# Kernel tuning notes

Hardware: AMD Instinct MI355X
Metric: run time of the kernel (lower is better)

The kernel has to match this reference:

```python
import jax, jax.numpy as jnp
import numpy as np
from jax import lax

EPS = 1e-05
Q = 4          # window size (hard-coded in BotBlock)
HEADS = 4
DIM = 16       # bottleneck(64) // heads(4)


def conv3x3(x, w, b):
    # x: [N,C,H,W], w: [O,I,3,3]
    y = lax.conv_general_dilated(x, w, (1, 1), ((1, 1), (1, 1)),
                                 dimension_numbers=('NCHW', 'OIHW', 'NCHW'))
    return y + b[None, :, None, None]


def batchnorm(x, gamma, beta):
    # training-mode BN: batch statistics over (N,H,W), biased variance
    m = jnp.mean(x, axis=(0, 2, 3), keepdims=True)
    v = jnp.var(x, axis=(0, 2, 3), keepdims=True)
    xn = (x - m) * lax.rsqrt(v + EPS)
    return xn * gamma[None, :, None, None] + beta[None, :, None, None]


def rel_to_abs(x):
    # x: [B, H, L, 2L-1] -> [B, H, L, L] via pad/reshape trick
    B, H, L, _ = x.shape
    x = jnp.pad(x, ((0, 0), (0, 0), (0, 0), (0, 1)))          # [B,H,L,2L]
    flat = x.reshape(B, H, -1)                                  # [B,H,2L*L]
    flat = jnp.pad(flat, ((0, 0), (0, 0), (0, L - 1)))
    final = flat.reshape(B, H, L + 1, 2 * L - 1)
    return final[:, :, :L, L - 1:]                              # [B,H,L,L]


def relative_logits_1d(q, rel_k, perm):
    # q: [b, n, h, w, d], rel_k: [2w-1, d]
    b, n, h, w, d = q.shape
    rl = jnp.einsum('bnhwd,md->bnhwm', q, rel_k)
    rl = rl.reshape(b, n * h, w, 2 * w - 1)
    rl = rel_to_abs(rl)                                         # [b, n*h, w, w]
    rl = rl.reshape(b, n, h, w, w)
    rl = jnp.broadcast_to(rl[:, :, :, None], (b, n, h, h, w, w))
    return jnp.transpose(rl, perm)


def rel_pos_attention(q, k, v, rel_w, rel_h):
    # q,k,v: [b, heads, h, w, d]
    b, n, h, w, d = q.shape
    q = q * (d ** -0.5)
    logits = jnp.einsum('bnhwd,bnpqd->bnhwpq', q, k)
    logits = logits + relative_logits_1d(q, rel_w, (0, 1, 2, 4, 3, 5))
    logits = logits + relative_logits_1d(jnp.transpose(q, (0, 1, 3, 2, 4)),
                                         rel_h, (0, 1, 4, 2, 5, 3))
    weights = jax.nn.softmax(logits.reshape(b, n, h, w, h * w), axis=-1)
    weights = weights.reshape(b, n, h, w, h, w)
    out = jnp.einsum('bnhwpq,bnpqd->bhwnd', weights, v)         # [b,h,w,n,d]
    return out.reshape(b, h, w, n * d)                          # fold heads


def setup_inputs() -> dict:
    key = jax.random.key(0)
    ks = jax.random.split(key, 16)
    C_in, C_bot, C_out = 64, 64, 256
    inp = {
        'x': jax.random.normal(ks[0], (2, C_in, 256, 256), jnp.float32),
        'conv1_w': jax.random.normal(ks[1], (C_bot, C_in, 3, 3), jnp.float32) * 0.05,
        'conv1_b': jnp.zeros((C_bot,), jnp.float32),
        'bn1_g': jnp.ones((C_bot,), jnp.float32),
        'bn1_b': jnp.zeros((C_bot,), jnp.float32),
        'wq': jax.random.normal(ks[2], (C_bot, HEADS, DIM), jnp.float32) * 0.01,
        'wk': jax.random.normal(ks[3], (C_bot, HEADS, DIM), jnp.float32) * 0.01,
        'wv': jax.random.normal(ks[4], (C_bot, HEADS, DIM), jnp.float32) * 0.01,
        'rel_w': jax.random.normal(ks[5], (2 * Q - 1, DIM), jnp.float32) * (DIM ** -0.5),
        'rel_h': jax.random.normal(ks[6], (2 * Q - 1, DIM), jnp.float32) * (DIM ** -0.5),
        'bn2_g': jnp.ones((C_bot,), jnp.float32),
        'bn2_b': jnp.zeros((C_bot,), jnp.float32),
        'conv3_w': jax.random.normal(ks[7], (C_out, C_bot, 3, 3), jnp.float32) * 0.05,
        'conv3_b': jnp.zeros((C_out,), jnp.float32),
        # NOTE: original init_zero=True zeros bn3 gamma; we randomize it so the
        # output (and gradients) are non-trivial for kernel correctness checks.
        'bn3_g': jax.random.normal(ks[8], (C_out,), jnp.float32),
        'bn3_b': jnp.zeros((C_out,), jnp.float32),
    }
    return inp


def reference(x, conv1_w, conv1_b, bn1_g, bn1_b, wq, wk, wv, rel_w, rel_h,
              bn2_g, bn2_b, conv3_w, conv3_b, bn3_g, bn3_b):
    N, C, H, W = x.shape
    P_h, P_w = H // Q, W // Q
    # raw memory reinterpretation into 4x4 blocks (matches torch .reshape)
    xb = x.reshape(N * P_h * P_w, C, Q, Q)
    out = jax.nn.relu(batchnorm(conv3x3(xb, conv1_w, conv1_b), bn1_g, bn1_b))
    # GroupPointWise projections: NCHW -> NHWC then einsum
    feat = jnp.transpose(out, (0, 2, 3, 1))                     # [b,h,w,c]
    q = jnp.einsum('bhwc,cnp->bnhwp', feat, wq)
    k = jnp.einsum('bhwc,cnp->bnhwp', feat, wk)
    v = jnp.einsum('bhwc,cnp->bnhwp', feat, wv)
    o = rel_pos_attention(q, k, v, rel_w, rel_h)                # [b,h,w,c]
    o = jnp.transpose(o, (0, 3, 1, 2))                          # NCHW
    o = jax.nn.relu(batchnorm(o, bn2_g, bn2_b))
    o = batchnorm(conv3x3(o, conv3_w, conv3_b), bn3_g, bn3_b)   # no act
    C1 = o.shape[1]
    o = o.reshape(N, C1, H, W)
    return jax.nn.relu(o)
```

## Files before the change

kernel.cpp:

```cpp
#include <hip/hip_runtime.h>
#include <stdint.h>


#define EPSV 1e-5f
#define INV_N (1.0f / 131072.0f)

typedef unsigned short u16;
typedef __attribute__((ext_vector_type(8))) short short8b;
typedef __attribute__((ext_vector_type(4))) float f32x4;

__device__ __forceinline__ u16 f2bf(float f) {
  unsigned u = __float_as_uint(f);
  u += 0x7fffu + ((u >> 16) & 1u);
  return (u16)(u >> 16);
}
__device__ __forceinline__ float bf2f(u16 h) {
  return __uint_as_float((unsigned)h << 16);
}

__device__ __forceinline__ float bn_scale(const float* __restrict__ acc,
                                          const float* __restrict__ gam,
                                          const float* __restrict__ bet,
                                          int C, int c, float& shift) {
  float S = acc[c], S2 = acc[C + c];
  float mean = S * INV_N;
  float var  = S2 * INV_N - mean * mean;
  float rstd = rsqrtf(var + EPSV);
  float sc = gam[c] * rstd;
  shift = bet[c] - mean * sc;
  return sc;
}

__global__ __launch_bounds__(256) void prep_kernel(const float* __restrict__ w1,
                                                   const float* __restrict__ w3,
                                                   const float* __restrict__ wq,
                                                   const float* __restrict__ wk,
                                                   const float* __restrict__ wv,
                                                   u16* __restrict__ wp1,
                                                   u16* __restrict__ wp3,
                                                   u16* __restrict__ wqkvT) {
  int i = blockIdx.x * 256 + threadIdx.x;
  const int tot1 = 18 * 64 * 40;
  const int tot3 = 9 * 256 * 64;
  if (i < tot1) {
    int ch = i / (64 * 40); int r = i - ch * 64 * 40; int o = r / 40; int kk = r - o * 40;
    float v = 0.f;
    if (kk < 32) { int k = ch * 32 + kk; int tap = k >> 6; int c = k & 63;
                   v = w1[o * 576 + c * 9 + tap]; }
    wp1[i] = f2bf(v);
  } else if (i < tot1 + tot3) {
    int j = i - tot1;
    int tap = j >> 14; int r = j & 16383; int o = r >> 6; int c = r & 63;
    wp3[j] = f2bf(w3[o * 576 + c * 9 + tap]);
  } else if (i < tot1 + tot3 + 192 * 64) {
    int j = i - tot1 - tot3;
    int oc = j >> 6, c = j & 63;
    const float* src = (oc < 64) ? wq : (oc < 128) ? wk : wv;
    wqkvT[j] = f2bf(src[(c << 6) + (oc & 63)]);
  }
}

__global__ __launch_bounds__(256) void conv1_kernel(const float* __restrict__ x,
                                                    const u16* __restrict__ wp,
                                                    u16* __restrict__ bufb,
                                                    float* __restrict__ partials1) {
  __shared__ __align__(16) char featA[257 * 128];
  __shared__ __align__(16) char ldsW[2][64 * 80];
  const int t = threadIdx.x;
  const int lane = t & 63, w = t >> 6;
  const int lrow = lane & 15, lk = lane >> 4;
  const int wm = w >> 1, wn = w & 1;
  const size_t Mbase = (size_t)blockIdx.x * 256;

  int rel[9];
  {
    const int pi = lrow >> 2, pj = lrow & 3;
#pragma unroll
    for (int tap = 0; tap < 9; ++tap) {
      const int ti = tap / 3, tj = tap - ti * 3;
      int si = pi + ti - 1, sj = pj + tj - 1;
      bool valid = ((unsigned)si < 4u) && ((unsigned)sj < 4u);
      rel[tap] = valid ? ((si * 4 + sj) << 7) : (1 << 24);
    }
  }

#pragma unroll
  for (int i = 0; i < 16; ++i) {
    float4 v = *reinterpret_cast<const float4*>(x + Mbase * 64 + i * 1024 + t * 4);
    const int c = t >> 2, p0 = (t & 3) * 4;
    float vv[4] = {v.x, v.y, v.z, v.w};
#pragma unroll
    for (int j = 0; j < 4; ++j) {
      int row = i * 16 + p0 + j;
      int byte = row * 128 + ((((c >> 3) ^ (row & 7)) << 4) | ((c & 7) << 1));
      *reinterpret_cast<u16*>(featA + byte) = f2bf(vv[j]);
    }
  }
  if (t < 8) *reinterpret_cast<uint4*>(featA + 256 * 128 + t * 16) = uint4{0, 0, 0, 0};

  uint4 s0, s1;
  {
    const u16* sp = wp;
    s0 = *reinterpret_cast<const uint4*>(sp + (size_t)t * 8);
    if (t < 64) s1 = *reinterpret_cast<const uint4*>(sp + (size_t)(t + 256) * 8);
    *reinterpret_cast<uint4*>(ldsW[0] + t * 16) = s0;
    if (t < 64) *reinterpret_cast<uint4*>(ldsW[0] + (t + 256) * 16) = s1;
  }
  __syncthreads();

  f32x4 acc[8][2] = {};
#pragma unroll
  for (int chn = 0; chn < 18; ++chn) {
    const int cur = chn & 1;
    const int tap = chn >> 1, kk = chn & 1;
    if (chn + 1 < 18) {
      const u16* sp = wp + (chn + 1) * 2560;
      s0 = *reinterpret_cast<const uint4*>(sp + (size_t)t * 8);
      if (t < 64) s1 = *reinterpret_cast<const uint4*>(sp + (size_t)(t + 256) * 8);
    }
    const int kkg = (kk << 6) | (lk << 4);
    short8b bw[2];
#pragma unroll
    for (int n = 0; n < 2; ++n)
      bw[n] = *reinterpret_cast<const short8b*>(ldsW[cur] + (wn * 32 + n * 16 + lrow) * 80 + lk * 16);
#pragma unroll
    for (int m = 0; m < 8; ++m) {
      int ad = ((wm * 128 + m * 16) << 7) + rel[tap];
      ad = ad < 32768 ? ad : 32768;
      ad += (kkg ^ ((ad >> 3) & 0x70));
      short8b af = *reinterpret_cast<const short8b*>(featA + ad);
#pragma unroll
      for (int n = 0; n < 2; ++n)
        acc[m][n] = __builtin_amdgcn_mfma_f32_16x16x32_bf16(af, bw[n], acc[m][n], 0, 0, 0);
    }
    if (chn + 1 < 18) {
      *reinterpret_cast<uint4*>(ldsW[cur ^ 1] + t * 16) = s0;
      if (t < 64) *reinterpret_cast<uint4*>(ldsW[cur ^ 1] + (t + 256) * 16) = s1;
    }
    __syncthreads();
  }

#pragma unroll
  for (int m = 0; m < 8; ++m) {
    const size_t rowg0 = Mbase + wm * 128 + m * 16 + lk * 4;
#pragma unroll
    for (int n = 0; n < 2; ++n) {
      const int o = wn * 32 + n * 16 + lrow;
#pragma unroll
      for (int r = 0; r < 4; ++r)
        bufb[(rowg0 + r) * 64 + o] = f2bf(acc[m][n][r]);
    }
  }

  float* pst = reinterpret_cast<float*>(featA);
  if (t < 128) pst[t] = 0.f;
  __syncthreads();
#pragma unroll
  for (int n = 0; n < 2; ++n) {
    float s = 0.f, s2 = 0.f;
#pragma unroll
    for (int m = 0; m < 8; ++m)
#pragma unroll
      for (int r = 0; r < 4; ++r) {
        float v = acc[m][n][r];
        s += v; s2 = fmaf(v, v, s2);
      }
    s += __shfl_xor(s, 16); s2 += __shfl_xor(s2, 16);
    s += __shfl_xor(s, 32); s2 += __shfl_xor(s2, 32);
    if (lk == 0) {
      const int o = wn * 32 + n * 16 + lrow;
      atomicAdd(&pst[o], s);
      atomicAdd(&pst[64 + o], s2);
    }
  }
  __syncthreads();
  if (t < 128) partials1[(size_t)blockIdx.x * 128 + t] = pst[t];
}

__global__ __launch_bounds__(256) void reduce12_kernel(const float* __restrict__ p,
                                                       float* __restrict__ acc, int nrows) {
  const int c = blockIdx.x, t = threadIdx.x;
  float s = 0.f;
  for (int i = t; i < nrows; i += 256) s += p[(size_t)i * 128 + c];
#pragma unroll
  for (int off = 32; off > 0; off >>= 1) s += __shfl_down(s, off);
  __shared__ float red[4];
  if ((t & 63) == 0) red[t >> 6] = s;
  __syncthreads();
  if (t == 0) acc[c] = red[0] + red[1] + red[2] + red[3];
}

__global__ __launch_bounds__(256) void attn_kernel(u16* __restrict__ buf,
                                                   const u16* __restrict__ wqkvT,
                                                   const float* __restrict__ relw,
                                                   const float* __restrict__ relh,
                                                   const float* __restrict__ acc1,
                                                   const float* __restrict__ g1,
                                                   const float* __restrict__ b1,
                                                   float* __restrict__ partials2) {
  __shared__ float scsh[64][2];
  __shared__ float pstA[128];
  __shared__ __align__(16) u16 feat_l[4][1024];
  __shared__ __align__(16) float qkvf[4][3264];
  const int t = threadIdx.x, u = t >> 6, lane = t & 63;
  const size_t b = (size_t)blockIdx.x * 4 + u;
  float* Wf = qkvf[u];

  if (t < 64) {
    float sh; float sc = bn_scale(acc1, g1, b1, 64, t, sh);
    scsh[t][0] = sc; scsh[t][1] = sh;
  }
  if (t < 128) pstA[t] = 0.f;
  __syncthreads();

  {
    const int pos = lane >> 2, cq = lane & 3;
    const u16* src = buf + b * 1024 + pos * 64 + cq * 16;
    short8b v0 = *reinterpret_cast<const short8b*>(src);
    short8b v1 = *reinterpret_cast<const short8b*>(src + 8);
    short8b p0, p1;
#pragma unroll
    for (int j = 0; j < 8; ++j) {
      const int c0 = cq * 16 + j, c1 = cq * 16 + 8 + j;
      p0[j] = (short)f2bf(fmaxf(fmaf(bf2f((u16)v0[j]), scsh[c0][0], scsh[c0][1]), 0.f));
      p1[j] = (short)f2bf(fmaxf(fmaf(bf2f((u16)v1[j]), scsh[c1][0], scsh[c1][1]), 0.f));
    }
    const int g0 = (cq * 2) ^ (pos & 7), g1g = (cq * 2 + 1) ^ (pos & 7);
    *reinterpret_cast<short8b*>(&feat_l[u][pos * 64 + g0 * 8]) = p0;
    *reinterpret_cast<short8b*>(&feat_l[u][pos * 64 + g1g * 8]) = p1;
  }

  const int dq = lane & 15, lk = lane >> 4;
  short8b afr[2];
#pragma unroll
  for (int ch = 0; ch < 2; ++ch) {
    const int kg = ch * 4 + lk;
    afr[ch] = *reinterpret_cast<const short8b*>(&feat_l[u][dq * 64 + ((kg ^ (dq & 7)) * 8)]);
  }
#pragma unroll
  for (int ct = 0; ct < 12; ++ct) {
    f32x4 d = {0.f, 0.f, 0.f, 0.f};
#pragma unroll
    for (int ch = 0; ch < 2; ++ch) {
      short8b bfr = *reinterpret_cast<const short8b*>(&wqkvT[(ct * 16 + dq) * 64 + ch * 32 + lk * 8]);
      d = __builtin_amdgcn_mfma_f32_16x16x32_bf16(afr[ch], bfr, d, 0, 0, 0);
    }
    if (ct < 4) {
      float* dst = Wf + ct * 280;
#pragma unroll
      for (int r = 0; r < 4; ++r) dst[(lk * 4 + r) * 17 + dq] = d[r] * 0.25f;
    } else {
      float* dst = (ct < 8) ? (Wf + 1120 + (ct - 4) * 264) : (Wf + 2176 + (ct - 8) * 264);
      const int cp = dq ^ (lk << 2);
#pragma unroll
      for (int r = 0; r < 4; ++r) dst[(lk * 4 + r) * 16 + cp] = d[r];
    }
  }

  const int n = lk, qp = dq;
  const int qi = qp >> 2, qj = qp & 3;
  float q_[16];
  {
    const float* qb = Wf + n * 280 + qp * 17;
#pragma unroll
    for (int d2 = 0; d2 < 16; ++d2) q_[d2] = qb[d2];
  }
  float rwq[4], rhq[4];
  {
    const float* rwp = relw + (3 - qj) * 16;
    const float* rhp = relh + (3 - qi) * 16;
#pragma unroll
    for (int m = 0; m < 4; ++m) {
      float a1 = 0.f, a2 = 0.f;
#pragma unroll
      for (int d2 = 0; d2 < 16; ++d2) {
        a1 = fmaf(q_[d2], rwp[m * 16 + d2], a1);
        a2 = fmaf(q_[d2], rhp[m * 16 + d2], a2);
      }
      rwq[m] = a1; rhq[m] = a2;
    }
  }
  float lo[16]; float mx = -1e30f;
  const float* kbase = Wf + 1120 + n * 264;
#pragma unroll
  for (int kp = 0; kp < 16; ++kp) {
    const float4* kr = reinterpret_cast<const float4*>(kbase + kp * 16);
    float s = rwq[kp & 3] + rhq[kp >> 2];
#pragma unroll
    for (int g = 0; g < 4; ++g) {
      float4 kv = kr[g];
      const int lg = (g ^ (kp >> 2)) * 4;
      s = fmaf(q_[lg], kv.x, s); s = fmaf(q_[lg + 1], kv.y, s);
      s = fmaf(q_[lg + 2], kv.z, s); s = fmaf(q_[lg + 3], kv.w, s);
    }
    lo[kp] = s; mx = fmaxf(mx, s);
  }
  float ssum = 0.f;
#pragma unroll
  for (int kp = 0; kp < 16; ++kp) { float e = __expf(lo[kp] - mx); lo[kp] = e; ssum += e; }
  const float inv = 1.0f / ssum;
  float ov[16];
#pragma unroll
  for (int j = 0; j < 16; ++j) ov[j] = 0.f;
  const float* vbase = Wf + 2176 + n * 264;
#pragma unroll
  for (int kp = 0; kp < 16; ++kp) {
    const float4* vr = reinterpret_cast<const float4*>(vbase + kp * 16);
    const float wgt = lo[kp];
#pragma unroll
    for (int g = 0; g < 4; ++g) {
      float4 vv = vr[g];
      const int lg = (g ^ (kp >> 2)) * 4;
      ov[lg] = fmaf(wgt, vv.x, ov[lg]);
      ov[lg + 1] = fmaf(wgt, vv.y, ov[lg + 1]);
      ov[lg + 2] = fmaf(wgt, vv.z, ov[lg + 2]);
      ov[lg + 3] = fmaf(wgt, vv.w, ov[lg + 3]);
    }
  }
#pragma unroll
  for (int j = 0; j < 16; ++j) ov[j] *= inv;

  {
    short8b o0, o1;
#pragma unroll
    for (int j = 0; j < 8; ++j) {
      o0[j] = (short)f2bf(ov[j]);
      o1[j] = (short)f2bf(ov[8 + j]);
    }
    u16* dstb = buf + b * 1024 + qp * 64 + (n << 4);
    *reinterpret_cast<short8b*>(dstb) = o0;
    *reinterpret_cast<short8b*>(dstb + 8) = o1;
  }

  {
    float* fl = Wf;
#pragma unroll
    for (int j = 0; j < 16; ++j) fl[qp * 69 + n * 16 + j] = ov[j];
    const int c = lane;
    float s = 0.f, s2 = 0.f;
#pragma unroll
    for (int pos = 0; pos < 16; ++pos) {
      float v = fl[pos * 69 + c];
      s += v; s2 = fmaf(v, v, s2);
    }
    atomicAdd(&pstA[c], s);
    atomicAdd(&pstA[64 + c], s2);
  }
  __syncthreads();
  if (t < 128) partials2[(size_t)blockIdx.x * 128 + t] = pstA[t];
}

__global__ __launch_bounds__(256, 2) void conv3_kernel(const u16* __restrict__ src,
                                                       const u16* __restrict__ wp,
                                                       const float* __restrict__ acc2,
                                                       const float* __restrict__ g2,
                                                       const float* __restrict__ b2,
                                                       u16* __restrict__ y3b,
                                                       float* __restrict__ partials3) {
  __shared__ __align__(16) u16 featB[257 * 64];
  __shared__ __align__(16) u16 ldsW[2][128 * 64];
  __shared__ float scsh[128];
  const int t = threadIdx.x;
  const int lane = t & 63, w = t >> 6;
  const int lrow = lane & 15, lk = lane >> 4;
  const int wm = w >> 1, wn = w & 1;
  const int Nbase = blockIdx.x * 256;
  const int ohalf = blockIdx.y;

  int rel[9];
  {
    const int pi = lrow >> 2, pj = lrow & 3;
#pragma unroll
    for (int tap = 0; tap < 9; ++tap) {
      const int ti = tap / 3, tj = tap - ti * 3;
      int si = pi + ti - 1, sj = pj + tj - 1;
      bool valid = ((unsigned)si < 4u) && ((unsigned)sj < 4u);
      rel[tap] = valid ? ((si * 4 + sj) << 7) : (1 << 24);
    }
  }

  if (t < 64) {
    float sh; float sc = bn_scale(acc2, g2, b2, 64, t, sh);
    scsh[t * 2] = sc; scsh[t * 2 + 1] = sh;
  }

  const int so = t >> 1, shalf = t & 1, so7 = so & 7;
  {
    const u16* wsrc = wp + ohalf * 8192 + so * 64 + shalf * 32;
    uint4 w0 = *reinterpret_cast<const uint4*>(wsrc);
    uint4 w1 = *reinterpret_cast<const uint4*>(wsrc + 8);
    uint4 w2 = *reinterpret_cast<const uint4*>(wsrc + 16);
    uint4 w3v = *reinterpret_cast<const uint4*>(wsrc + 24);
    char* dst = (char*)ldsW[0] + so * 128;
    const int gb = shalf * 4;
    *reinterpret_cast<uint4*>(dst + (((gb + 0) ^ so7) << 4)) = w0;
    *reinterpret_cast<uint4*>(dst + (((gb + 1) ^ so7) << 4)) = w1;
    *reinterpret_cast<uint4*>(dst + (((gb + 2) ^ so7) << 4)) = w2;
    *reinterpret_cast<uint4*>(dst + (((gb + 3) ^ so7) << 4)) = w3v;
  }
  __syncthreads();

  {
    const u16* srow = src + (size_t)(Nbase + t) * 64;
    char* drow = (char*)featB + t * 128;
    const int r7 = t & 7;
#pragma unroll
    for (int g = 0; g < 8; ++g) {
      short8b v = *reinterpret_cast<const short8b*>(srow + g * 8);
      short8b pk;
#pragma unroll
      for (int j = 0; j < 8; ++j) {
        const int c = g * 8 + j;
        pk[j] = (short)f2bf(fmaxf(fmaf(bf2f((u16)v[j]), scsh[c * 2], scsh[c * 2 + 1]), 0.f));
      }
      *reinterpret_cast<short8b*>(drow + ((g ^ r7) << 4)) = pk;
    }
  }
  if (t < 8) *reinterpret_cast<uint4*>((char*)featB + 32768 + t * 16) = uint4{0, 0, 0, 0};

  uint4 r0, r1, r2, r3v;
  {
    const u16* wsrc = wp + 16384 + ohalf * 8192 + so * 64 + shalf * 32;
    r0 = *reinterpret_cast<const uint4*>(wsrc);
    r1 = *reinterpret_cast<const uint4*>(wsrc + 8);
    r2 = *reinterpret_cast<const uint4*>(wsrc + 16);
    r3v = *reinterpret_cast<const uint4*>(wsrc + 24);
  }
  __syncthreads();

  f32x4 acc[4][8] = {};
  const char* fB = (const char*)featB;
  const int swzA0 = (lk << 4) ^ ((lrow & 7) << 4);
  const int swzA1 = (64 | (lk << 4)) ^ ((lrow & 7) << 4);

#pragma unroll
  for (int tap = 0; tap < 9; ++tap) {
    const int cur = tap & 1;
    const char* lW = (const char*)ldsW[cur];
    short8b aw0[4], aw1[4];
#pragma unroll
    for (int m = 0; m < 4; ++m) {
      const int rowoff = (wm * 64 + m * 16 + lrow) << 7;
      aw0[m] = *reinterpret_cast<const short8b*>(lW + rowoff + swzA0);
      aw1[m] = *reinterpret_cast<const short8b*>(lW + rowoff + swzA1);
    }
#pragma unroll
    for (int n = 0; n < 8; ++n) {
      int ad0 = ((wn * 128 + n * 16) << 7) + rel[tap];
      ad0 = ad0 < 32768 ? ad0 : 32768;
      const int swz = (ad0 >> 3) & 0x70;
      short8b bf0 = *reinterpret_cast<const short8b*>(fB + ad0 + ((lk << 4) ^ swz));
      short8b bf1 = *reinterpret_cast<const short8b*>(fB + ad0 + ((64 | (lk << 4)) ^ swz));
#pragma unroll
      for (int m = 0; m < 4; ++m) {
        acc[m][n] = __builtin_amdgcn_mfma_f32_16x16x32_bf16(aw0[m], bf0, acc[m][n], 0, 0, 0);
        acc[m][n] = __builtin_amdgcn_mfma_f32_16x16x32_bf16(aw1[m], bf1, acc[m][n], 0, 0, 0);
      }
    }
    if (tap < 8) {
      char* dst = (char*)ldsW[cur ^ 1] + so * 128;
      const int gb = shalf * 4;
      *reinterpret_cast<uint4*>(dst + (((gb + 0) ^ so7) << 4)) = r0;
      *reinterpret_cast<uint4*>(dst + (((gb + 1) ^ so7) << 4)) = r1;
      *reinterpret_cast<uint4*>(dst + (((gb + 2) ^ so7) << 4)) = r2;
      *reinterpret_cast<uint4*>(dst + (((gb + 3) ^ so7) << 4)) = r3v;
      if (tap < 7) {
        const u16* wsrc = wp + (tap + 2) * 16384 + ohalf * 8192 + so * 64 + shalf * 32;
        r0 = *reinterpret_cast<const uint4*>(wsrc);
        r1 = *reinterpret_cast<const uint4*>(wsrc + 8);
        r2 = *reinterpret_cast<const uint4*>(wsrc + 16);
        r3v = *reinterpret_cast<const uint4*>(wsrc + 24);
      }
    }
    __syncthreads();
  }

#pragma unroll
  for (int m = 0; m < 4; ++m) {
    const int o = ohalf * 128 + wm * 64 + m * 16 + lk * 4;
#pragma unroll
    for (int n = 0; n < 8; ++n) {
      const int colg = Nbase + wn * 128 + n * 16 + lrow;
      const int b = colg >> 4, p = colg & 15;
      u16* dst = y3b + (size_t)b * 4096 + (size_t)o * 16 + p;
#pragma unroll
      for (int r = 0; r < 4; ++r)
        dst[r * 16] = f2bf(acc[m][n][r]);
    }
  }

  float* pst = reinterpret_cast<float*>(featB);
  pst[t] = 0.f;
  __syncthreads();
#pragma unroll
  for (int m = 0; m < 4; ++m) {
#pragma unroll
    for (int r = 0; r < 4; ++r) {
      float s = 0.f, s2 = 0.f;
#pragma unroll
      for (int n = 0; n < 8; ++n) {
        float v = acc[m][n][r];
        s += v; s2 = fmaf(v, v, s2);
      }
      s += __shfl_xor(s, 1); s2 += __shfl_xor(s2, 1);
      s += __shfl_xor(s, 2); s2 += __shfl_xor(s2, 2);
      s += __shfl_xor(s, 4); s2 += __shfl_xor(s2, 4);
      s += __shfl_xor(s, 8); s2 += __shfl_xor(s2, 8);
      if (lrow == 0) {
        const int ch = wm * 64 + m * 16 + lk * 4 + r;
        atomicAdd(&pst[ch], s);
        atomicAdd(&pst[128 + ch], s2);
      }
    }
  }
  __syncthreads();
  partials3[((size_t)(ohalf * 512 + blockIdx.x)) * 256 + t] = pst[t];
}

__global__ __launch_bounds__(256) void reduce3_kernel(const float* __restrict__ p,
                                                      float* __restrict__ acc3) {
  const int c2 = blockIdx.x, t = threadIdx.x;
  const int kind = c2 >> 8, c = c2 & 255;
  const int h = c >> 7, chl = c & 127;
  float s = 0.f;
  for (int i = t; i < 512; i += 256)
    s += p[((size_t)(h * 512 + i)) * 256 + kind * 128 + chl];
#pragma unroll
  for (int off = 32; off > 0; off >>= 1) s += __shfl_down(s, off);
  __shared__ float red[4];
  if ((t & 63) == 0) red[t >> 6] = s;
  __syncthreads();
  if (t == 0) acc3[kind * 256 + c] = red[0] + red[1] + red[2] + red[3];
}

__global__ __launch_bounds__(256) void final_kernel(const u16* __restrict__ y3b,
                                                    float* __restrict__ out,
                                                    const float* __restrict__ acc3,
                                                    const float* __restrict__ g3,
                                                    const float* __restrict__ b3) {
  const size_t i = ((size_t)blockIdx.x * 256 + threadIdx.x) * 8;
  const int c = (int)((i >> 4) & 255);
  float sh; const float sc = bn_scale(acc3, g3, b3, 256, c, sh);
  short8b v = *reinterpret_cast<const short8b*>(y3b + i);
  float4 o0, o1;
  o0.x = fmaxf(fmaf(bf2f((u16)v[0]), sc, sh), 0.f);
  o0.y = fmaxf(fmaf(bf2f((u16)v[1]), sc, sh), 0.f);
  o0.z = fmaxf(fmaf(bf2f((u16)v[2]), sc, sh), 0.f);
  o0.w = fmaxf(fmaf(bf2f((u16)v[3]), sc, sh), 0.f);
  o1.x = fmaxf(fmaf(bf2f((u16)v[4]), sc, sh), 0.f);
  o1.y = fmaxf(fmaf(bf2f((u16)v[5]), sc, sh), 0.f);
  o1.z = fmaxf(fmaf(bf2f((u16)v[6]), sc, sh), 0.f);
  o1.w = fmaxf(fmaf(bf2f((u16)v[7]), sc, sh), 0.f);
  *reinterpret_cast<float4*>(out + i) = o0;
  *reinterpret_cast<float4*>(out + i + 4) = o1;
}

extern "C" void kernel_launch(void* const* d_in, const int* in_sizes, int n_in,
                              void* d_out, int out_size, void* d_ws, size_t ws_size,
                              hipStream_t stream) {
  const float* x   = (const float*)d_in[0];
  const float* w1  = (const float*)d_in[1];
  const float* g1  = (const float*)d_in[3];
  const float* bb1 = (const float*)d_in[4];
  const float* wq  = (const float*)d_in[5];
  const float* wk  = (const float*)d_in[6];
  const float* wv  = (const float*)d_in[7];
  const float* rw  = (const float*)d_in[8];
  const float* rh  = (const float*)d_in[9];
  const float* g2  = (const float*)d_in[10];
  const float* bb2 = (const float*)d_in[11];
  const float* w3  = (const float*)d_in[12];
  const float* g3  = (const float*)d_in[14];
  const float* bb3 = (const float*)d_in[15];
  float* out = (float*)d_out;
  float* ws  = (float*)d_ws;

  u16*   bufb   = (u16*)ws;
  u16*   y3b    = bufb + 8388608;
  u16*   wp1    = y3b + 33554432;
  u16*   wp3    = wp1 + 46080;
  u16*   wqkvT  = wp3 + 147456;
  float* acc1   = ws + 21074432;
  float* acc2   = acc1 + 128;
  float* acc3   = acc2 + 128;
  float* part1  = acc3 + 512;
  float* part2  = part1 + 65536;
  float* part3  = part2 + 262144;

  prep_kernel<<<804, 256, 0, stream>>>(w1, w3, wq, wk, wv, wp1, wp3, wqkvT);
  conv1_kernel<<<512, 256, 0, stream>>>(x, wp1, bufb, part1);
  reduce12_kernel<<<128, 256, 0, stream>>>(part1, acc1, 512);
  attn_kernel<<<2048, 256, 0, stream>>>(bufb, wqkvT, rw, rh, acc1, g1, bb1, part2);
  reduce12_kernel<<<128, 256, 0, stream>>>(part2, acc2, 2048);
  conv3_kernel<<<dim3(512, 2), 256, 0, stream>>>(bufb, wp3, acc2, g2, bb2, y3b, part3);
  reduce3_kernel<<<512, 256, 0, stream>>>(part3, acc3);
  final_kernel<<<16384, 256, 0, stream>>>(y3b, out, acc3, g3, bb3);
}
```

Measured before the change: 163.9 us.

## Fuse conv3, BN3 reduction and final epilogue into a cooperative kernel

```diff
diff --git a/kernel.cpp b/kernel.cpp
--- a/kernel.cpp
+++ b/kernel.cpp
@@ -1,4 +1,5 @@
 #include <hip/hip_runtime.h>
+#include <hip/hip_cooperative_groups.h>
 #include <stdint.h>
 
 
@@ -16,6 +17,11 @@
 }
 __device__ __forceinline__ float bf2f(u16 h) {
   return __uint_as_float((unsigned)h << 16);
+}
+__device__ __forceinline__ unsigned cvtpk(float lo, float hi) {
+  unsigned r;
+  asm("v_cvt_pk_bf16_f32 %0, %1, %2" : "=v"(r) : "v"(lo), "v"(hi));
+  return r;
 }
 
 __device__ __forceinline__ float bn_scale(const float* __restrict__ acc,
@@ -36,6 +42,8 @@
                                                    const float* __restrict__ wq,
                                                    const float* __restrict__ wk,
                                                    const float* __restrict__ wv,
+                                                   const float* __restrict__ relw,
+                                                   const float* __restrict__ relh,
                                                    u16* __restrict__ wp1,
                                                    u16* __restrict__ wp3,
                                                    u16* __restrict__ wqkvT) {
@@ -57,6 +65,17 @@
     int oc = j >> 6, c = j & 63;
     const float* src = (oc < 64) ? wq : (oc < 128) ? wk : wv;
     wqkvT[j] = f2bf(src[(c << 6) + (oc & 63)]);
+  } else if (i < tot1 + tot3 + 192 * 64 + 4096) {
+    int j = i - tot1 - tot3 - 192 * 64;
+    int c = j & 63; int col = (j >> 6) & 31; int tbl = j >> 11;
+    int n = col >> 3, m = col & 7;
+    float v = 0.f;
+    if (m < 7) {
+      const float* rel = tbl ? relh : relw;
+#pragma unroll
+      for (int d = 0; d < 16; ++d) v += wq[c * 64 + n * 16 + d] * rel[m * 16 + d];
+    }
+    wqkvT[(192 + tbl * 32 + col) * 64 + c] = f2bf(v);
   }
 }
 
@@ -84,16 +103,21 @@
     }
   }
 
-#pragma unroll
-  for (int i = 0; i < 16; ++i) {
-    float4 v = *reinterpret_cast<const float4*>(x + Mbase * 64 + i * 1024 + t * 4);
-    const int c = t >> 2, p0 = (t & 3) * 4;
-    float vv[4] = {v.x, v.y, v.z, v.w};
-#pragma unroll
-    for (int j = 0; j < 4; ++j) {
-      int row = i * 16 + p0 + j;
-      int byte = row * 128 + ((((c >> 3) ^ (row & 7)) << 4) | ((c & 7) << 1));
-      *reinterpret_cast<u16*>(featA + byte) = f2bf(vv[j]);
+  {
+    const int cp = t >> 3, ph = t & 7;
+    const int gsw = ((cp >> 2) << 4) | ((cp & 3) << 2);
+#pragma unroll
+    for (int i = 0; i < 16; ++i) {
+      const float* bp = x + Mbase * 64 + i * 1024 + cp * 32 + ph * 2;
+      float2 a = *reinterpret_cast<const float2*>(bp);
+      float2 b = *reinterpret_cast<const float2*>(bp + 16);
+#pragma unroll
+      for (int j = 0; j < 2; ++j) {
+        const int row = i * 16 + ph * 2 + j;
+        unsigned pk = cvtpk(j ? a.y : a.x, j ? b.y : b.x);
+        const int byte = row * 128 + (gsw ^ ((row & 7) << 4));
+        *reinterpret_cast<unsigned*>(featA + byte) = pk;
+      }
     }
   }
   if (t < 8) *reinterpret_cast<uint4*>(featA + 256 * 128 + t * 16) = uint4{0, 0, 0, 0};
@@ -192,8 +216,6 @@
 
 __global__ __launch_bounds__(256) void attn_kernel(u16* __restrict__ buf,
                                                    const u16* __restrict__ wqkvT,
-                                                   const float* __restrict__ relw,
-                                                   const float* __restrict__ relh,
                                                    const float* __restrict__ acc1,
                                                    const float* __restrict__ g1,
                                                    const float* __restrict__ b1,
@@ -201,10 +223,12 @@
   __shared__ float scsh[64][2];
   __shared__ float pstA[128];
   __shared__ __align__(16) u16 feat_l[4][1024];
-  __shared__ __align__(16) float qkvf[4][3264];
+  __shared__ __align__(16) float qkvf[4][3200];
+  __shared__ __align__(16) float relLs[4][1152];
   const int t = threadIdx.x, u = t >> 6, lane = t & 63;
   const size_t b = (size_t)blockIdx.x * 4 + u;
   float* Wf = qkvf[u];
+  float* rL = relLs[u];
 
   if (t < 64) {
     float sh; float sc = bn_scale(acc1, g1, b1, 64, t, sh);
@@ -218,16 +242,18 @@
     const u16* src = buf + b * 1024 + pos * 64 + cq * 16;
     short8b v0 = *reinterpret_cast<const short8b*>(src);
     short8b v1 = *reinterpret_cast<const short8b*>(src + 8);
-    short8b p0, p1;
+    float f[16];
 #pragma unroll
     for (int j = 0; j < 8; ++j) {
       const int c0 = cq * 16 + j, c1 = cq * 16 + 8 + j;
-      p0[j] = (short)f2bf(fmaxf(fmaf(bf2f((u16)v0[j]), scsh[c0][0], scsh[c0][1]), 0.f));
-      p1[j] = (short)f2bf(fmaxf(fmaf(bf2f((u16)v1[j]), scsh[c1][0], scsh[c1][1]), 0.f));
-    }
+      f[j]     = fmaxf(fmaf(bf2f((u16)v0[j]), scsh[c0][0], scsh[c0][1]), 0.f);
+      f[8 + j] = fmaxf(fmaf(bf2f((u16)v1[j]), scsh[c1][0], scsh[c1][1]), 0.f);
+    }
+    uint4 q0{cvtpk(f[0], f[1]), cvtpk(f[2], f[3]), cvtpk(f[4], f[5]), cvtpk(f[6], f[7])};
+    uint4 q1{cvtpk(f[8], f[9]), cvtpk(f[10], f[11]), cvtpk(f[12], f[13]), cvtpk(f[14], f[15])};
     const int g0 = (cq * 2) ^ (pos & 7), g1g = (cq * 2 + 1) ^ (pos & 7);
-    *reinterpret_cast<short8b*>(&feat_l[u][pos * 64 + g0 * 8]) = p0;
-    *reinterpret_cast<short8b*>(&feat_l[u][pos * 64 + g1g * 8]) = p1;
+    *reinterpret_cast<uint4*>(&feat_l[u][pos * 64 + g0 * 8]) = q0;
+    *reinterpret_cast<uint4*>(&feat_l[u][pos * 64 + g1g * 8]) = q1;
   }
 
   const int dq = lane & 15, lk = lane >> 4;
@@ -238,7 +264,7 @@
     afr[ch] = *reinterpret_cast<const short8b*>(&feat_l[u][dq * 64 + ((kg ^ (dq & 7)) * 8)]);
   }
 #pragma unroll
-  for (int ct = 0; ct < 12; ++ct) {
+  for (int ct = 0; ct < 16; ++ct) {
     f32x4 d = {0.f, 0.f, 0.f, 0.f};
 #pragma unroll
     for (int ch = 0; ch < 2; ++ch) {
@@ -246,14 +272,20 @@
       d = __builtin_amdgcn_mfma_f32_16x16x32_bf16(afr[ch], bfr, d, 0, 0, 0);
     }
     if (ct < 4) {
-      float* dst = Wf + ct * 280;
+      float* dst = Wf + ct * 272;
 #pragma unroll
       for (int r = 0; r < 4; ++r) dst[(lk * 4 + r) * 17 + dq] = d[r] * 0.25f;
+    } else if (ct < 12) {
+      float* dst = (ct < 8) ? (Wf + 1088 + (ct - 4) * 264) : (Wf + 2144 + (ct - 8) * 264);
+      const int cp = dq ^ (lk << 2);
+#pragma unroll
+      for (int r = 0; r < 4; ++r) dst[(lk * 4 + r) * 16 + cp] = d[r];
     } else {
-      float* dst = (ct < 8) ? (Wf + 1120 + (ct - 4) * 264) : (Wf + 2176 + (ct - 8) * 264);
-      const int cp = dq ^ (lk << 2);
-#pragma unroll
-      for (int r = 0; r < 4; ++r) dst[(lk * 4 + r) * 16 + cp] = d[r];
+      const int rc = ct - 12, tbl = rc >> 1;
+      const int nn = ((rc & 1) << 1) | (dq >> 3), mm = dq & 7;
+      float* dst = rL + tbl * 576 + nn * 144 + mm;
+#pragma unroll
+      for (int r = 0; r < 4; ++r) dst[(lk * 4 + r) * 9] = d[r] * 0.25f;
     }
   }
 
@@ -261,27 +293,19 @@
   const int qi = qp >> 2, qj = qp & 3;
   float q_[16];
   {
-    const float* qb = Wf + n * 280 + qp * 17;
+    const float* qb = Wf + n * 272 + qp * 17;
 #pragma unroll
     for (int d2 = 0; d2 < 16; ++d2) q_[d2] = qb[d2];
   }
   float rwq[4], rhq[4];
   {
-    const float* rwp = relw + (3 - qj) * 16;
-    const float* rhp = relh + (3 - qi) * 16;
-#pragma unroll
-    for (int m = 0; m < 4; ++m) {
-      float a1 = 0.f, a2 = 0.f;
-#pragma unroll
-      for (int d2 = 0; d2 < 16; ++d2) {
-        a1 = fmaf(q_[d2], rwp[m * 16 + d2], a1);
-        a2 = fmaf(q_[d2], rhp[m * 16 + d2], a2);
-      }
-      rwq[m] = a1; rhq[m] = a2;
-    }
+    const float* rw = rL + n * 144 + qp * 9 + (3 - qj);
+    const float* rh = rL + 576 + n * 144 + qp * 9 + (3 - qi);
+#pragma unroll
+    for (int k = 0; k < 4; ++k) { rwq[k] = rw[k]; rhq[k] = rh[k]; }
   }
   float lo[16]; float mx = -1e30f;
-  const float* kbase = Wf + 1120 + n * 264;
+  const float* kbase = Wf + 1088 + n * 264;
 #pragma unroll
   for (int kp = 0; kp < 16; ++kp) {
     const float4* kr = reinterpret_cast<const float4*>(kbase + kp * 16);
@@ -302,7 +326,7 @@
   float ov[16];
 #pragma unroll
   for (int j = 0; j < 16; ++j) ov[j] = 0.f;
-  const float* vbase = Wf + 2176 + n * 264;
+  const float* vbase = Wf + 2144 + n * 264;
 #pragma unroll
   for (int kp = 0; kp < 16; ++kp) {
     const float4* vr = reinterpret_cast<const float4*>(vbase + kp * 16);
@@ -321,15 +345,11 @@
   for (int j = 0; j < 16; ++j) ov[j] *= inv;
 
   {
-    short8b o0, o1;
-#pragma unroll
-    for (int j = 0; j < 8; ++j) {
-      o0[j] = (short)f2bf(ov[j]);
-      o1[j] = (short)f2bf(ov[8 + j]);
-    }
+    uint4 o0{cvtpk(ov[0], ov[1]), cvtpk(ov[2], ov[3]), cvtpk(ov[4], ov[5]), cvtpk(ov[6], ov[7])};
+    uint4 o1{cvtpk(ov[8], ov[9]), cvtpk(ov[10], ov[11]), cvtpk(ov[12], ov[13]), cvtpk(ov[14], ov[15])};
     u16* dstb = buf + b * 1024 + qp * 64 + (n << 4);
-    *reinterpret_cast<short8b*>(dstb) = o0;
-    *reinterpret_cast<short8b*>(dstb + 8) = o1;
+    *reinterpret_cast<uint4*>(dstb) = o0;
+    *reinterpret_cast<uint4*>(dstb + 8) = o1;
   }
 
   {
@@ -348,6 +368,250 @@
   }
   __syncthreads();
   if (t < 128) partials2[(size_t)blockIdx.x * 128 + t] = pstA[t];
+}
+
+__global__ __launch_bounds__(256, 2) void conv3_coop(const u16* __restrict__ src,
+                                                     const u16* __restrict__ wp,
+                                                     const float* __restrict__ acc2,
+                                                     const float* __restrict__ g2,
+                                                     const float* __restrict__ b2,
+                                                     const float* __restrict__ g3,
+                                                     const float* __restrict__ b3,
+                                                     float* __restrict__ out,
+                                                     u16* __restrict__ y3a,
+                                                     float* __restrict__ p3,
+                                                     float* __restrict__ acc3) {
+  __shared__ __align__(16) u16 featB[257 * 64];
+  __shared__ __align__(16) u16 ldsW[2][128 * 64];
+  __shared__ float scsh[128];
+  __shared__ float pst[256];
+  const int t = threadIdx.x, wg = blockIdx.x;
+  const int lane = t & 63, w = t >> 6;
+  const int lrow = lane & 15, lk = lane >> 4;
+  const int wm = w >> 1, wn = w & 1;
+  const int Nbase = wg * 256;
+
+  int rel[9];
+  {
+    const int pi = lrow >> 2, pj = lrow & 3;
+#pragma unroll
+    for (int tap = 0; tap < 9; ++tap) {
+      const int ti = tap / 3, tj = tap - ti * 3;
+      int si = pi + ti - 1, sj = pj + tj - 1;
+      bool valid = ((unsigned)si < 4u) && ((unsigned)sj < 4u);
+      rel[tap] = valid ? ((si * 4 + sj) << 7) : (1 << 24);
+    }
+  }
+
+  if (t < 64) {
+    float sh; float sc = bn_scale(acc2, g2, b2, 64, t, sh);
+    scsh[t * 2] = sc; scsh[t * 2 + 1] = sh;
+  }
+
+  const int so = t >> 1, shalf = t & 1, so7 = so & 7;
+  {
+    const u16* wsrc = wp + so * 64 + shalf * 32;
+    uint4 w0 = *reinterpret_cast<const uint4*>(wsrc);
+    uint4 w1 = *reinterpret_cast<const uint4*>(wsrc + 8);
+    uint4 w2 = *reinterpret_cast<const uint4*>(wsrc + 16);
+    uint4 w3v = *reinterpret_cast<const uint4*>(wsrc + 24);
+    char* dst = (char*)ldsW[0] + so * 128;
+    const int gb = shalf * 4;
+    *reinterpret_cast<uint4*>(dst + (((gb + 0) ^ so7) << 4)) = w0;
+    *reinterpret_cast<uint4*>(dst + (((gb + 1) ^ so7) << 4)) = w1;
+    *reinterpret_cast<uint4*>(dst + (((gb + 2) ^ so7) << 4)) = w2;
+    *reinterpret_cast<uint4*>(dst + (((gb + 3) ^ so7) << 4)) = w3v;
+  }
+  __syncthreads();
+
+  {
+    const u16* srow = src + (size_t)(Nbase + t) * 64;
+    char* drow = (char*)featB + t * 128;
+    const int r7 = t & 7;
+#pragma unroll
+    for (int g = 0; g < 8; ++g) {
+      short8b v = *reinterpret_cast<const short8b*>(srow + g * 8);
+      float f[8];
+#pragma unroll
+      for (int j = 0; j < 8; ++j) {
+        const int c = g * 8 + j;
+        f[j] = fmaxf(fmaf(bf2f((u16)v[j]), scsh[c * 2], scsh[c * 2 + 1]), 0.f);
+      }
+      uint4 pk{cvtpk(f[0], f[1]), cvtpk(f[2], f[3]), cvtpk(f[4], f[5]), cvtpk(f[6], f[7])};
+      *reinterpret_cast<uint4*>(drow + ((g ^ r7) << 4)) = pk;
+    }
+  }
+  if (t < 8) *reinterpret_cast<uint4*>((char*)featB + 32768 + t * 16) = uint4{0, 0, 0, 0};
+
+  const char* fB = (const char*)featB;
+  const int swzA0 = (lk << 4) ^ ((lrow & 7) << 4);
+  const int swzA1 = (64 | (lk << 4)) ^ ((lrow & 7) << 4);
+
+  f32x4 acc[4][8];
+  for (int oh = 0; oh < 2; ++oh) {
+    uint4 r0, r1, r2, r3v;
+    {
+      const u16* wsrc = wp + 16384 + oh * 8192 + so * 64 + shalf * 32;
+      r0 = *reinterpret_cast<const uint4*>(wsrc);
+      r1 = *reinterpret_cast<const uint4*>(wsrc + 8);
+      r2 = *reinterpret_cast<const uint4*>(wsrc + 16);
+      r3v = *reinterpret_cast<const uint4*>(wsrc + 24);
+    }
+    if (oh == 1) {
+      const u16* wsrc = wp + 8192 + so * 64 + shalf * 32;
+      uint4 w0 = *reinterpret_cast<const uint4*>(wsrc);
+      uint4 w1 = *reinterpret_cast<const uint4*>(wsrc + 8);
+      uint4 w2 = *reinterpret_cast<const uint4*>(wsrc + 16);
+      uint4 w3w = *reinterpret_cast<const uint4*>(wsrc + 24);
+      char* dst = (char*)ldsW[0] + so * 128;
+      const int gb = shalf * 4;
+      *reinterpret_cast<uint4*>(dst + (((gb + 0) ^ so7) << 4)) = w0;
+      *reinterpret_cast<uint4*>(dst + (((gb + 1) ^ so7) << 4)) = w1;
+      *reinterpret_cast<uint4*>(dst + (((gb + 2) ^ so7) << 4)) = w2;
+      *reinterpret_cast<uint4*>(dst + (((gb + 3) ^ so7) << 4)) = w3w;
+    }
+#pragma unroll
+    for (int m = 0; m < 4; ++m)
+#pragma unroll
+      for (int n = 0; n < 8; ++n) acc[m][n] = f32x4{0.f, 0.f, 0.f, 0.f};
+    __syncthreads();
+
+#pragma unroll
+    for (int tap = 0; tap < 9; ++tap) {
+      const int cur = tap & 1;
+      const char* lW = (const char*)ldsW[cur];
+      short8b aw0[4], aw1[4];
+#pragma unroll
+      for (int m = 0; m < 4; ++m) {
+        const int rowoff = (wm * 64 + m * 16 + lrow) << 7;
+        aw0[m] = *reinterpret_cast<const short8b*>(lW + rowoff + swzA0);
+        aw1[m] = *reinterpret_cast<const short8b*>(lW + rowoff + swzA1);
+      }
+#pragma unroll
+      for (int n = 0; n < 8; ++n) {
+        int ad0 = ((wn * 128 + n * 16) << 7) + rel[tap];
+        ad0 = ad0 < 32768 ? ad0 : 32768;
+        const int swz = (ad0 >> 3) & 0x70;
+        short8b bf0 = *reinterpret_cast<const short8b*>(fB + ad0 + ((lk << 4) ^ swz));
+        short8b bf1 = *reinterpret_cast<const short8b*>(fB + ad0 + ((64 | (lk << 4)) ^ swz));
+#pragma unroll
+        for (int m = 0; m < 4; ++m) {
+          acc[m][n] = __builtin_amdgcn_mfma_f32_16x16x32_bf16(aw0[m], bf0, acc[m][n], 0, 0, 0);
+          acc[m][n] = __builtin_amdgcn_mfma_f32_16x16x32_bf16(aw1[m], bf1, acc[m][n], 0, 0, 0);
+        }
+      }
+      if (tap < 8) {
+        char* dst = (char*)ldsW[cur ^ 1] + so * 128;
+        const int gb = shalf * 4;
+        *reinterpret_cast<uint4*>(dst + (((gb + 0) ^ so7) << 4)) = r0;
+        *reinterpret_cast<uint4*>(dst + (((gb + 1) ^ so7) << 4)) = r1;
+        *reinterpret_cast<uint4*>(dst + (((gb + 2) ^ so7) << 4)) = r2;
+        *reinterpret_cast<uint4*>(dst + (((gb + 3) ^ so7) << 4)) = r3v;
+        if (tap < 7) {
+          const u16* wsrc = wp + (tap + 2) * 16384 + oh * 8192 + so * 64 + shalf * 32;
+          r0 = *reinterpret_cast<const uint4*>(wsrc);
+          r1 = *reinterpret_cast<const uint4*>(wsrc + 8);
+          r2 = *reinterpret_cast<const uint4*>(wsrc + 16);
+          r3v = *reinterpret_cast<const uint4*>(wsrc + 24);
+        }
+      }
+      __syncthreads();
+    }
+
+    if (oh == 0) {
+#pragma unroll
+      for (int m = 0; m < 4; ++m) {
+        const int ol = wm * 64 + m * 16 + lk * 4;
+#pragma unroll
+        for (int n = 0; n < 8; ++n) {
+          const int col = wn * 128 + n * 16 + lrow;
+          u16* dst = y3a + (size_t)wg * 32768 + (size_t)ol * 256 + col;
+#pragma unroll
+          for (int r = 0; r < 4; ++r) dst[r * 256] = f2bf(acc[m][n][r]);
+        }
+      }
+    }
+    pst[t] = 0.f;
+    __syncthreads();
+#pragma unroll
+    for (int m = 0; m < 4; ++m) {
+#pragma unroll
+      for (int r = 0; r < 4; ++r) {
+        float s = 0.f, s2 = 0.f;
+#pragma unroll
+        for (int n = 0; n < 8; ++n) {
+          float v = acc[m][n][r];
+          s += v; s2 = fmaf(v, v, s2);
+        }
+        s += __shfl_xor(s, 1); s2 += __shfl_xor(s2, 1);
+        s += __shfl_xor(s, 2); s2 += __shfl_xor(s2, 2);
+        s += __shfl_xor(s, 4); s2 += __shfl_xor(s2, 4);
+        s += __shfl_xor(s, 8); s2 += __shfl_xor(s2, 8);
+        if (lrow == 0) {
+          const int ch = wm * 64 + m * 16 + lk * 4 + r;
+          atomicAdd(&pst[ch], s);
+          atomicAdd(&pst[128 + ch], s2);
+        }
+      }
+    }
+    __syncthreads();
+    p3[(size_t)wg * 512 + oh * 256 + t] = pst[t];
+    __syncthreads();
+  }
+
+  __threadfence();
+  cooperative_groups::this_grid().sync();
+
+  {
+    const int idx = wg;
+    float s = p3[(size_t)t * 512 + idx] + p3[(size_t)(t + 256) * 512 + idx];
+#pragma unroll
+    for (int off = 32; off > 0; off >>= 1) s += __shfl_down(s, off);
+    if (lane == 0) pst[w] = s;
+    __syncthreads();
+    if (t == 0) {
+      const int half = idx >> 8, kind = (idx >> 7) & 1, chl = idx & 127;
+      acc3[kind * 256 + half * 128 + chl] = pst[0] + pst[1] + pst[2] + pst[3];
+    }
+  }
+  __threadfence();
+  cooperative_groups::this_grid().sync();
+
+#pragma unroll
+  for (int m = 0; m < 4; ++m) {
+#pragma unroll
+    for (int r = 0; r < 4; ++r) {
+      const int o = 128 + wm * 64 + m * 16 + lk * 4 + r;
+      float sh; const float sc = bn_scale(acc3, g3, b3, 256, o, sh);
+#pragma unroll
+      for (int n = 0; n < 8; ++n) {
+        const int colg = Nbase + wn * 128 + n * 16 + lrow;
+        out[(size_t)(colg >> 4) * 4096 + o * 16 + (colg & 15)] =
+            fmaxf(fmaf(acc[m][n][r], sc, sh), 0.f);
+      }
+    }
+  }
+  {
+    const int o = t >> 1, p8 = (t & 1) * 8;
+    float sh; const float sc = bn_scale(acc3, g3, b3, 256, o, sh);
+    const u16* srcA = y3a + (size_t)wg * 32768 + (size_t)o * 256;
+#pragma unroll
+    for (int bb = 0; bb < 16; ++bb) {
+      short8b v = *reinterpret_cast<const short8b*>(srcA + bb * 16 + p8);
+      float4 f0, f1;
+      f0.x = fmaxf(fmaf(bf2f((u16)v[0]), sc, sh), 0.f);
+      f0.y = fmaxf(fmaf(bf2f((u16)v[1]), sc, sh), 0.f);
+      f0.z = fmaxf(fmaf(bf2f((u16)v[2]), sc, sh), 0.f);
+      f0.w = fmaxf(fmaf(bf2f((u16)v[3]), sc, sh), 0.f);
+      f1.x = fmaxf(fmaf(bf2f((u16)v[4]), sc, sh), 0.f);
+      f1.y = fmaxf(fmaf(bf2f((u16)v[5]), sc, sh), 0.f);
+      f1.z = fmaxf(fmaf(bf2f((u16)v[6]), sc, sh), 0.f);
+      f1.w = fmaxf(fmaf(bf2f((u16)v[7]), sc, sh), 0.f);
+      float* dsto = out + (size_t)(wg * 16 + bb) * 4096 + o * 16 + p8;
+      *reinterpret_cast<float4*>(dsto) = f0;
+      *reinterpret_cast<float4*>(dsto + 4) = f1;
+    }
+  }
 }
 
 __global__ __launch_bounds__(256, 2) void conv3_kernel(const u16* __restrict__ src,
@@ -378,12 +642,10 @@
       rel[tap] = valid ? ((si * 4 + sj) << 7) : (1 << 24);
     }
   }
-
   if (t < 64) {
     float sh; float sc = bn_scale(acc2, g2, b2, 64, t, sh);
     scsh[t * 2] = sc; scsh[t * 2 + 1] = sh;
   }
-
   const int so = t >> 1, shalf = t & 1, so7 = so & 7;
   {
     const u16* wsrc = wp + ohalf * 8192 + so * 64 + shalf * 32;
@@ -399,7 +661,6 @@
     *reinterpret_cast<uint4*>(dst + (((gb + 3) ^ so7) << 4)) = w3v;
   }
   __syncthreads();
-
   {
     const u16* srow = src + (size_t)(Nbase + t) * 64;
     char* drow = (char*)featB + t * 128;
@@ -407,17 +668,17 @@
 #pragma unroll
     for (int g = 0; g < 8; ++g) {
       short8b v = *reinterpret_cast<const short8b*>(srow + g * 8);
-      short8b pk;
+      float f[8];
 #pragma unroll
       for (int j = 0; j < 8; ++j) {
         const int c = g * 8 + j;
-        pk[j] = (short)f2bf(fmaxf(fmaf(bf2f((u16)v[j]), scsh[c * 2], scsh[c * 2 + 1]), 0.f));
-      }
-      *reinterpret_cast<short8b*>(drow + ((g ^ r7) << 4)) = pk;
+        f[j] = fmaxf(fmaf(bf2f((u16)v[j]), scsh[c * 2], scsh[c * 2 + 1]), 0.f);
+      }
+      uint4 pk{cvtpk(f[0], f[1]), cvtpk(f[2], f[3]), cvtpk(f[4], f[5]), cvtpk(f[6], f[7])};
+      *reinterpret_cast<uint4*>(drow + ((g ^ r7) << 4)) = pk;
     }
   }
   if (t < 8) *reinterpret_cast<uint4*>((char*)featB + 32768 + t * 16) = uint4{0, 0, 0, 0};
-
   uint4 r0, r1, r2, r3v;
   {
     const u16* wsrc = wp + 16384 + ohalf * 8192 + so * 64 + shalf * 32;
@@ -427,12 +688,10 @@
     r3v = *reinterpret_cast<const uint4*>(wsrc + 24);
   }
   __syncthreads();
-
   f32x4 acc[4][8] = {};
   const char* fB = (const char*)featB;
   const int swzA0 = (lk << 4) ^ ((lrow & 7) << 4);
   const int swzA1 = (64 | (lk << 4)) ^ ((lrow & 7) << 4);
-
 #pragma unroll
   for (int tap = 0; tap < 9; ++tap) {
     const int cur = tap & 1;
@@ -474,7 +733,6 @@
     }
     __syncthreads();
   }
-
 #pragma unroll
   for (int m = 0; m < 4; ++m) {
     const int o = ohalf * 128 + wm * 64 + m * 16 + lk * 4;
@@ -484,11 +742,9 @@
       const int b = colg >> 4, p = colg & 15;
       u16* dst = y3b + (size_t)b * 4096 + (size_t)o * 16 + p;
 #pragma unroll
-      for (int r = 0; r < 4; ++r)
-        dst[r * 16] = f2bf(acc[m][n][r]);
-    }
-  }
-
+      for (int r = 0; r < 4; ++r) dst[r * 16] = f2bf(acc[m][n][r]);
+    }
+  }
   float* pst = reinterpret_cast<float*>(featB);
   pst[t] = 0.f;
   __syncthreads();
@@ -576,23 +832,35 @@
   float* ws  = (float*)d_ws;
 
   u16*   bufb   = (u16*)ws;
-  u16*   y3b    = bufb + 8388608;
-  u16*   wp1    = y3b + 33554432;
+  u16*   y3     = bufb + 8388608;
+  u16*   wp1    = y3 + 33554432;
   u16*   wp3    = wp1 + 46080;
   u16*   wqkvT  = wp3 + 147456;
-  float* acc1   = ws + 21074432;
+  float* acc1   = ws + 21076480;
   float* acc2   = acc1 + 128;
   float* acc3   = acc2 + 128;
   float* part1  = acc3 + 512;
   float* part2  = part1 + 65536;
   float* part3  = part2 + 262144;
 
-  prep_kernel<<<804, 256, 0, stream>>>(w1, w3, wq, wk, wv, wp1, wp3, wqkvT);
+  prep_kernel<<<820, 256, 0, stream>>>(w1, w3, wq, wk, wv, rw, rh, wp1, wp3, wqkvT);
   conv1_kernel<<<512, 256, 0, stream>>>(x, wp1, bufb, part1);
   reduce12_kernel<<<128, 256, 0, stream>>>(part1, acc1, 512);
-  attn_kernel<<<2048, 256, 0, stream>>>(bufb, wqkvT, rw, rh, acc1, g1, bb1, part2);
+  attn_kernel<<<2048, 256, 0, stream>>>(bufb, wqkvT, acc1, g1, bb1, part2);
   reduce12_kernel<<<128, 256, 0, stream>>>(part2, acc2, 2048);
-  conv3_kernel<<<dim3(512, 2), 256, 0, stream>>>(bufb, wp3, acc2, g2, bb2, y3b, part3);
-  reduce3_kernel<<<512, 256, 0, stream>>>(part3, acc3);
-  final_kernel<<<16384, 256, 0, stream>>>(y3b, out, acc3, g3, bb3);
-}
+
+  {
+    const u16* srcb = bufb; const u16* wpc = wp3;
+    void* args[] = {(void*)&srcb, (void*)&wpc, (void*)&acc2, (void*)&g2, (void*)&bb2,
+                    (void*)&g3, (void*)&bb3, (void*)&out, (void*)&y3, (void*)&part3,
+                    (void*)&acc3};
+    hipError_t e = hipLaunchCooperativeKernel((const void*)conv3_coop, dim3(512), dim3(256),
+                                              args, 0, stream);
+    if (e != hipSuccess) {
+      (void)hipGetLastError();
+      conv3_kernel<<<dim3(512, 2), 256, 0, stream>>>(bufb, wp3, acc2, g2, bb2, y3, part3);
+      reduce3_kernel<<<512, 256, 0, stream>>>(part3, acc3);
+      final_kernel<<<16384, 256, 0, stream>>>(y3, out, acc3, g3, bb3);
+    }
+  }
+}
```

After: 444.5 us. 171% more time.
